# Performance work log

Measured on AMD Instinct MI355X. Metric: run time of the kernel, lower is better.

## Reference

```python
import jax, jax.numpy as jnp
import numpy as np

N = 50000
E = 600000
LLM_DIM = 640
HIDDEN = 128
STRUCT_DIM = 16
N_STRUCT_TYPES = 5
N_LAYERS = 2
LN_EPS = 1e-5


def setup_inputs() -> dict:
    key = jax.random.key(0)
    ks = jax.random.split(key, 10)
    llm_feat = jax.random.normal(ks[0], (N, LLM_DIM), dtype=jnp.float32)
    struct_type_ids = jax.random.randint(ks[1], (N,), 0, N_STRUCT_TYPES, dtype=jnp.int64)
    edge_index = jax.random.randint(ks[2], (2, E), 0, N, dtype=jnp.int64)
    proj_out = HIDDEN - STRUCT_DIM  # 112
    proj_W = jax.random.normal(ks[3], (LLM_DIM, proj_out), dtype=jnp.float32) / np.sqrt(LLM_DIM)
    proj_b = jnp.zeros((proj_out,), dtype=jnp.float32)
    struct_emb = jax.random.normal(ks[4], (N_STRUCT_TYPES, STRUCT_DIM), dtype=jnp.float32)
    gcn_W = jax.random.normal(ks[5], (N_LAYERS, HIDDEN, HIDDEN), dtype=jnp.float32) / np.sqrt(HIDDEN)
    gcn_b = jnp.zeros((N_LAYERS, HIDDEN), dtype=jnp.float32)
    ln_g = jnp.ones((HIDDEN,), dtype=jnp.float32)
    ln_b = jnp.zeros((HIDDEN,), dtype=jnp.float32)
    return dict(llm_feat=llm_feat, struct_type_ids=struct_type_ids, edge_index=edge_index,
                proj_W=proj_W, proj_b=proj_b, struct_emb=struct_emb,
                gcn_W=gcn_W, gcn_b=gcn_b, ln_g=ln_g, ln_b=ln_b)


def _gcn_conv(x, src, dst, deg_inv_sqrt, W, b):
    """PyG GCNConv: x' = D^{-1/2}(A+I)D^{-1/2} (x W) + b, D over A+I."""
    xw = x @ W  # [N, H]
    norm = deg_inv_sqrt[src] * deg_inv_sqrt[dst]  # [E]
    msg = xw[src] * norm[:, None]  # [E, H]
    agg = jax.ops.segment_sum(msg, dst, num_segments=N)  # [N, H]
    # self-loop contribution: norm_ii = deg_i^{-1}
    agg = agg + xw * (deg_inv_sqrt * deg_inv_sqrt)[:, None]
    return agg + b


def reference(llm_feat, struct_type_ids, edge_index, proj_W, proj_b,
              struct_emb, gcn_W, gcn_b, ln_g, ln_b):
    x_llm = llm_feat @ proj_W + proj_b  # [N, hidden-struct_dim]
    x_struct = struct_emb[struct_type_ids]  # [N, struct_dim]
    x = jnp.concatenate([x_llm, x_struct], axis=-1)  # [N, hidden]

    src, dst = edge_index[0], edge_index[1]
    # degree with self-loops (A + I)
    deg = 1.0 + jax.ops.segment_sum(jnp.ones((E,), dtype=x.dtype), dst, num_segments=N)
    deg_inv_sqrt = jax.lax.rsqrt(deg)

    for l in range(N_LAYERS):
        x_new = jax.nn.relu(_gcn_conv(x, src, dst, deg_inv_sqrt, gcn_W[l], gcn_b[l]))
        # dropout is identity in eval mode
        x = x + x_new

    mean = jnp.mean(x, axis=-1, keepdims=True)
    var = jnp.mean(jnp.square(x - mean), axis=-1, keepdims=True)
    return (x - mean) * jax.lax.rsqrt(var + LN_EPS) * ln_g + ln_b
```

## Files before the change

### kernel.cpp

```cpp
#include <hip/hip_runtime.h>

#define N_NODES 50000
#define E_EDGES 600000
#define LLM_DIM 640
#define HIDDEN 128
#define POUT 112
#define NB_SCAN 98
#define FILL_BLOCKS 2344
#define CONV_ELEMS (POUT * LLM_DIM + 2 * HIDDEN * HIDDEN)
#define CONV_BLOCKS 408

typedef __attribute__((ext_vector_type(8))) short bf16x8;
typedef __attribute__((ext_vector_type(4))) float f32x4;

__device__ inline unsigned short f2bf(float f) {
    unsigned u = __float_as_uint(f);
    u += 0x7fff + ((u >> 16) & 1);
    return (unsigned short)(u >> 16);
}
__device__ inline float bflo(unsigned v) { return __uint_as_float(v << 16); }
__device__ inline float bfhi(unsigned v) { return __uint_as_float(v & 0xffff0000u); }

__global__ void deg_count(const int* __restrict__ eidx, int* __restrict__ cnt) {
    int e = blockIdx.x * 256 + threadIdx.x;
    if (e < E_EDGES) atomicAdd(&cnt[eidx[E_EDGES + e]], 1);
}

__global__ __launch_bounds__(256) void scan_blocksum(const int* __restrict__ cnt, int* __restrict__ bsum,
                                                     float* __restrict__ dis) {
    __shared__ int s[256];
    int b = blockIdx.x, t = threadIdx.x;
    int i0 = b * 512 + t, i1 = i0 + 256;
    int c0 = (i0 < N_NODES ? cnt[i0] : 0);
    int c1 = (i1 < N_NODES ? cnt[i1] : 0);
    if (i0 < N_NODES) dis[i0] = rsqrtf(1.0f + (float)c0);
    if (i1 < N_NODES) dis[i1] = rsqrtf(1.0f + (float)c1);
    s[t] = c0 + c1;
    __syncthreads();
    for (int st = 128; st; st >>= 1) {
        if (t < st) s[t] += s[t + st];
        __syncthreads();
    }
    if (t == 0) bsum[b] = s[0];
}

__global__ void scan_bsum(const int* __restrict__ bsum, int* __restrict__ bpre) {
    __shared__ int s[128];
    int t = threadIdx.x;
    if (t < NB_SCAN) s[t] = bsum[t];
    __syncthreads();
    if (t == 0) {
        int a = 0;
        for (int i = 0; i < NB_SCAN; i++) { int v = s[i]; s[i] = a; a += v; }
    }
    __syncthreads();
    if (t < NB_SCAN) bpre[t] = s[t];
}

__global__ __launch_bounds__(256) void scan_offs(const int* __restrict__ cnt, const int* __restrict__ bpre,
                                                 int* __restrict__ offs) {
    __shared__ int sA[512], sB[512];
    int b = blockIdx.x, t = threadIdx.x;
    int i0 = b * 512 + t, i1 = i0 + 256;
    int v0 = (i0 < N_NODES ? cnt[i0] : 0);
    int v1 = (i1 < N_NODES ? cnt[i1] : 0);
    sA[t] = v0; sA[t + 256] = v1;
    int* src = sA; int* dst = sB;
    for (int st = 1; st < 512; st <<= 1) {
        __syncthreads();
        dst[t]       = src[t]       + (t       >= st ? src[t - st]       : 0);
        dst[t + 256] = src[t + 256] + (t + 256 >= st ? src[t + 256 - st] : 0);
        int* tmp = src; src = dst; dst = tmp;
    }
    __syncthreads();
    int base = bpre[b];
    if (i0 < N_NODES) offs[i0] = base + src[t] - v0;
    if (i1 < N_NODES) offs[i1] = base + src[t + 256] - v1;
    if (b == 0 && t == 0) offs[N_NODES] = E_EDGES;
}

__global__ void fill_and_conv(const int* __restrict__ eidx, const int* __restrict__ offs,
                              int* __restrict__ pos, int* __restrict__ srcs,
                              const float* __restrict__ Wp, const float* __restrict__ Wg,
                              unsigned short* __restrict__ Wt, unsigned short* __restrict__ Wt2) {
    int b = blockIdx.x;
    if (b < FILL_BLOCKS) {
        int e = b * 256 + threadIdx.x;
        if (e >= E_EDGES) return;
        int s = eidx[e];
        int d = eidx[E_EDGES + e];
        int p = atomicAdd(&pos[d], 1);
        srcs[offs[d] + p] = s;
    } else {
        int idx = (b - FILL_BLOCKS) * 256 + threadIdx.x;
        if (idx < POUT * LLM_DIM) {
            int n = idx / LLM_DIM;
            int k = idx - n * LLM_DIM;
            Wt[(size_t)n * LLM_DIM + k] = f2bf(Wp[(size_t)k * POUT + n]);
        } else if (idx < CONV_ELEMS) {
            int i2 = idx - POUT * LLM_DIM;
            int l = i2 >> 14;
            int rem = i2 & 16383;
            int n = rem >> 7;
            int k = rem & 127;
            Wt2[i2] = f2bf(Wg[l * 16384 + k * 128 + n]);
        }
    }
}

__global__ __launch_bounds__(256) void proj_mfma(const float* __restrict__ A,
                                                 const unsigned short* __restrict__ Wt,
                                                 const float* __restrict__ bias,
                                                 const float* __restrict__ emb,
                                                 const int* __restrict__ sid,
                                                 const float* __restrict__ dis,
                                                 unsigned short* __restrict__ Xs) {
    __shared__ short As[64][72];
    __shared__ short Bs[112][72];
    const int tid = threadIdx.x;
    const int wave = tid >> 6, lane = tid & 63;
    const int row0 = blockIdx.x * 64;
    const int l15 = lane & 15, l4 = lane >> 4;

    f32x4 acc[7];
#pragma unroll
    for (int j = 0; j < 7; j++) acc[j] = (f32x4){0.f, 0.f, 0.f, 0.f};

    for (int k0 = 0; k0 < LLM_DIM; k0 += 64) {
#pragma unroll
        for (int i = 0; i < 4; i++) {
            int f = i * 256 + tid;
            int r = f >> 4;
            int q = f & 15;
            int grow = row0 + r;
            float4 v = make_float4(0.f, 0.f, 0.f, 0.f);
            if (grow < N_NODES)
                v = *reinterpret_cast<const float4*>(A + (size_t)grow * LLM_DIM + k0 + q * 4);
            uint2 u;
            u.x = (unsigned)f2bf(v.x) | ((unsigned)f2bf(v.y) << 16);
            u.y = (unsigned)f2bf(v.z) | ((unsigned)f2bf(v.w) << 16);
            *reinterpret_cast<uint2*>(&As[r][q * 4]) = u;
        }
#pragma unroll
        for (int i = 0; i < 7; i++) {
            int f = i * 256 + tid;
            int n = f >> 4;
            int q = f & 15;
            uint2 v = *reinterpret_cast<const uint2*>(Wt + (size_t)n * LLM_DIM + k0 + q * 4);
            *reinterpret_cast<uint2*>(&Bs[n][q * 4]) = v;
        }
        __syncthreads();
#pragma unroll
        for (int ks = 0; ks < 2; ks++) {
            int kk = ks * 32 + l4 * 8;
            bf16x8 a = *reinterpret_cast<bf16x8*>(&As[wave * 16 + l15][kk]);
#pragma unroll
            for (int ct = 0; ct < 7; ct++) {
                bf16x8 b = *reinterpret_cast<bf16x8*>(&Bs[ct * 16 + l15][kk]);
                acc[ct] = __builtin_amdgcn_mfma_f32_16x16x32_bf16(a, b, acc[ct], 0, 0, 0);
            }
        }
        __syncthreads();
    }
#pragma unroll
    for (int r = 0; r < 4; r++) {
        int row = row0 + wave * 16 + l4 * 4 + r;
        if (row >= N_NODES) continue;
        float d = dis[row];
#pragma unroll
        for (int ct = 0; ct < 7; ct++) {
            int col = ct * 16 + l15;
            Xs[(size_t)row * HIDDEN + col] = f2bf(d * (acc[ct][r] + bias[col]));
        }
        float e = emb[sid[row] * 16 + l15];
        Xs[(size_t)row * HIDDEN + POUT + l15] = f2bf(d * e);
    }
}

__global__ __launch_bounds__(256) void gather(const unsigned short* __restrict__ Xs,
                                              const int* __restrict__ offs,
                                              const int* __restrict__ srcs,
                                              const float* __restrict__ dis,
                                              unsigned short* __restrict__ Gb) {
    int node = blockIdx.x * 4 + (threadIdx.x >> 6);
    int lane = threadIdx.x & 63;
    if (node >= N_NODES) return;
    int beg = __builtin_amdgcn_readfirstlane(offs[node]);
    int end = __builtin_amdgcn_readfirstlane(offs[node + 1]);
    const unsigned* X32 = reinterpret_cast<const unsigned*>(Xs);
    float d = dis[node];
    unsigned sv = X32[(size_t)node * 64 + lane];
    float ax = 0.f, ay = 0.f;
    int e = beg;
    while (e < end) {
        int n = end - e;
        if (n > 64) n = 64;
        int idx = (lane < n) ? srcs[e + lane] : 0;
        int j = 0;
        for (; j + 8 <= n; j += 8) {
            int s0 = __shfl(idx, j);
            int s1 = __shfl(idx, j + 1);
            int s2 = __shfl(idx, j + 2);
            int s3 = __shfl(idx, j + 3);
            int s4 = __shfl(idx, j + 4);
            int s5 = __shfl(idx, j + 5);
            int s6 = __shfl(idx, j + 6);
            int s7 = __shfl(idx, j + 7);
            unsigned v0 = X32[(size_t)s0 * 64 + lane];
            unsigned v1 = X32[(size_t)s1 * 64 + lane];
            unsigned v2 = X32[(size_t)s2 * 64 + lane];
            unsigned v3 = X32[(size_t)s3 * 64 + lane];
            unsigned v4 = X32[(size_t)s4 * 64 + lane];
            unsigned v5 = X32[(size_t)s5 * 64 + lane];
            unsigned v6 = X32[(size_t)s6 * 64 + lane];
            unsigned v7 = X32[(size_t)s7 * 64 + lane];
            ax += ((bflo(v0) + bflo(v1)) + (bflo(v2) + bflo(v3)))
                + ((bflo(v4) + bflo(v5)) + (bflo(v6) + bflo(v7)));
            ay += ((bfhi(v0) + bfhi(v1)) + (bfhi(v2) + bfhi(v3)))
                + ((bfhi(v4) + bfhi(v5)) + (bfhi(v6) + bfhi(v7)));
        }
        if (j + 4 <= n) {
            int s0 = __shfl(idx, j);
            int s1 = __shfl(idx, j + 1);
            int s2 = __shfl(idx, j + 2);
            int s3 = __shfl(idx, j + 3);
            unsigned v0 = X32[(size_t)s0 * 64 + lane];
            unsigned v1 = X32[(size_t)s1 * 64 + lane];
            unsigned v2 = X32[(size_t)s2 * 64 + lane];
            unsigned v3 = X32[(size_t)s3 * 64 + lane];
            ax += (bflo(v0) + bflo(v1)) + (bflo(v2) + bflo(v3));
            ay += (bfhi(v0) + bfhi(v1)) + (bfhi(v2) + bfhi(v3));
            j += 4;
        }
        int rem = n - j;
        if (rem > 0) {
            int s0 = __shfl(idx, j);
            int s1 = __shfl(idx, j + (rem > 1 ? 1 : 0));
            int s2 = __shfl(idx, j + (rem > 2 ? 2 : 0));
            unsigned v0 = X32[(size_t)s0 * 64 + lane];
            unsigned v1 = X32[(size_t)s1 * 64 + lane];
            unsigned v2 = X32[(size_t)s2 * 64 + lane];
            ax += bflo(v0) + (rem > 1 ? bflo(v1) : 0.f) + (rem > 2 ? bflo(v2) : 0.f);
            ay += bfhi(v0) + (rem > 1 ? bfhi(v1) : 0.f) + (rem > 2 ? bfhi(v2) : 0.f);
        }
        e += 64;
    }
    ax = d * (ax + bflo(sv));
    ay = d * (ay + bfhi(sv));
    reinterpret_cast<unsigned*>(Gb)[(size_t)node * 64 + lane] =
        (unsigned)f2bf(ax) | ((unsigned)f2bf(ay) << 16);
}

template <int MODE>
__global__ __launch_bounds__(256) void gemm_fin(const unsigned short* __restrict__ Gb,
                                                const unsigned short* __restrict__ Wt2,
                                                const float* __restrict__ bias,
                                                const float* __restrict__ dis,
                                                const float* __restrict__ lng,
                                                const float* __restrict__ lnb,
                                                const unsigned short* XsIn,
                                                float* __restrict__ X,
                                                unsigned short* XsOut) {
    __shared__ short As[64][136];
    __shared__ short Bs[128][136];
    const int tid = threadIdx.x;
    const int wave = tid >> 6, lane = tid & 63;
    const int row0 = blockIdx.x * 64;
    const int l15 = lane & 15, l4 = lane >> 4;

#pragma unroll
    for (int i = 0; i < 4; i++) {
        int f = i * 256 + tid;
        int r = f >> 4;
        int q = f & 15;
        int grow = row0 + r;
        uint4 v = make_uint4(0, 0, 0, 0);
        if (grow < N_NODES)
            v = reinterpret_cast<const uint4*>(Gb + (size_t)grow * HIDDEN)[q];
        *reinterpret_cast<uint4*>(&As[r][q * 8]) = v;
    }
#pragma unroll
    for (int i = 0; i < 8; i++) {
        int f = i * 256 + tid;
        int r = f >> 4;
        int q = f & 15;
        uint4 v = reinterpret_cast<const uint4*>(Wt2 + (size_t)r * HIDDEN)[q];
        *reinterpret_cast<uint4*>(&Bs[r][q * 8]) = v;
    }

    const unsigned* XsU = reinterpret_cast<const unsigned*>(XsIn);
    float xs[8][4];
    float dv[4];
#pragma unroll
    for (int r = 0; r < 4; r++) {
        int row = row0 + wave * 16 + l4 * 4 + r;
        int rc = row < N_NODES ? row : 0;
        dv[r] = dis[rc];
        bool hi = (l15 & 1) != 0;
#pragma unroll
        for (int ct = 0; ct < 8; ct++) {
            unsigned u = XsU[(size_t)rc * 64 + ct * 8 + (l15 >> 1)];
            xs[ct][r] = hi ? bfhi(u) : bflo(u);
        }
    }

    __syncthreads();

    f32x4 acc[8];
#pragma unroll
    for (int j = 0; j < 8; j++) acc[j] = (f32x4){0.f, 0.f, 0.f, 0.f};
#pragma unroll
    for (int ks = 0; ks < 4; ks++) {
        int kk = ks * 32 + l4 * 8;
        bf16x8 a = *reinterpret_cast<bf16x8*>(&As[wave * 16 + l15][kk]);
#pragma unroll
        for (int ct = 0; ct < 8; ct++) {
            bf16x8 b = *reinterpret_cast<bf16x8*>(&Bs[ct * 16 + l15][kk]);
            acc[ct] = __builtin_amdgcn_mfma_f32_16x16x32_bf16(a, b, acc[ct], 0, 0, 0);
        }
    }

    float bcol[8];
#pragma unroll
    for (int ct = 0; ct < 8; ct++) bcol[ct] = bias[ct * 16 + l15];

    float vv[8][4];
#pragma unroll
    for (int r = 0; r < 4; r++) {
#pragma unroll
        for (int ct = 0; ct < 8; ct++)
            vv[ct][r] = xs[ct][r] + dv[r] * fmaxf(acc[ct][r] + bcol[ct], 0.f);
    }

    if (MODE == 0) {
#pragma unroll
        for (int r = 0; r < 4; r++) {
            int row = row0 + wave * 16 + l4 * 4 + r;
            if (row >= N_NODES) continue;
#pragma unroll
            for (int ct = 0; ct < 8; ct++)
                XsOut[(size_t)row * HIDDEN + ct * 16 + l15] = f2bf(vv[ct][r]);
        }
    } else {
        float s[4], q2[4];
#pragma unroll
        for (int r = 0; r < 4; r++) {
            s[r] = 0.f; q2[r] = 0.f;
#pragma unroll
            for (int ct = 0; ct < 8; ct++) {
                s[r] += vv[ct][r];
                q2[r] += vv[ct][r] * vv[ct][r];
            }
        }
#pragma unroll
        for (int off = 1; off < 16; off <<= 1) {
#pragma unroll
            for (int r = 0; r < 4; r++) {
                s[r] += __shfl_xor(s[r], off);
                q2[r] += __shfl_xor(q2[r], off);
            }
        }
        float gcol[8], bcol2[8];
#pragma unroll
        for (int ct = 0; ct < 8; ct++) {
            gcol[ct] = lng[ct * 16 + l15];
            bcol2[ct] = lnb[ct * 16 + l15];
        }
#pragma unroll
        for (int r = 0; r < 4; r++) {
            int row = row0 + wave * 16 + l4 * 4 + r;
            if (row >= N_NODES) continue;
            float mean = s[r] * (1.f / 128.f);
            float var = q2[r] * (1.f / 128.f) - mean * mean;
            float inv = rsqrtf(var + 1e-5f * dv[r] * dv[r]);
#pragma unroll
            for (int ct = 0; ct < 8; ct++) {
                int col = ct * 16 + l15;
                X[(size_t)row * HIDDEN + col] = (vv[ct][r] - mean) * inv * gcol[ct] + bcol2[ct];
            }
        }
    }
}

extern "C" void kernel_launch(void* const* d_in, const int* in_sizes, int n_in,
                              void* d_out, int out_size, void* d_ws, size_t ws_size,
                              hipStream_t stream) {
    const float* llm   = (const float*)d_in[0];
    const int*   sid   = (const int*)d_in[1];
    const int*   eidx  = (const int*)d_in[2];
    const float* projW = (const float*)d_in[3];
    const float* projb = (const float*)d_in[4];
    const float* emb   = (const float*)d_in[5];
    const float* gcnW  = (const float*)d_in[6];
    const float* gcnb  = (const float*)d_in[7];
    const float* lng   = (const float*)d_in[8];
    const float* lnb   = (const float*)d_in[9];

    float* X = (float*)d_out;
    unsigned short* Xs = (unsigned short*)d_ws;
    unsigned short* Gb = Xs + (size_t)N_NODES * HIDDEN;
    unsigned short* Wt = Gb;
    unsigned short* Wt2 = Gb + (size_t)N_NODES * HIDDEN;
    float* dis = (float*)(Wt2 + 2 * HIDDEN * HIDDEN);
    int* cnt  = (int*)(dis + N_NODES);
    int* pos  = cnt + N_NODES;
    int* offs = pos + N_NODES;
    int* bsum = offs + N_NODES + 1;
    int* bpre = bsum + 128;
    int* srcs = bpre + 128;

    hipMemsetAsync(cnt, 0, 2 * N_NODES * sizeof(int), stream);
    deg_count<<<FILL_BLOCKS, 256, 0, stream>>>(eidx, cnt);
    scan_blocksum<<<NB_SCAN, 256, 0, stream>>>(cnt, bsum, dis);
    scan_bsum<<<1, 128, 0, stream>>>(bsum, bpre);
    scan_offs<<<NB_SCAN, 256, 0, stream>>>(cnt, bpre, offs);
    fill_and_conv<<<FILL_BLOCKS + CONV_BLOCKS, 256, 0, stream>>>(eidx, offs, pos, srcs,
                                                                 projW, gcnW, Wt, Wt2);

    proj_mfma<<<(N_NODES + 63) / 64, 256, 0, stream>>>(llm, Wt, projb, emb, sid, dis, Xs);

    gather<<<(N_NODES + 3) / 4, 256, 0, stream>>>(Xs, offs, srcs, dis, Gb);
    gemm_fin<0><<<(N_NODES + 63) / 64, 256, 0, stream>>>(Gb, Wt2, gcnb, dis, lng, lnb, Xs, X, Xs);
    gather<<<(N_NODES + 3) / 4, 256, 0, stream>>>(Xs, offs, srcs, dis, Gb);
    gemm_fin<1><<<(N_NODES + 63) / 64, 256, 0, stream>>>(Gb, Wt2 + HIDDEN * HIDDEN, gcnb + HIDDEN,
                                                         dis, lng, lnb, Xs, X, Xs);
}
```

Baseline: 364.5 us.

## Fuse CSR preprocessing kernels into one cooperative kernel with grid syncs

Replaces the memset plus five preprocessing kernels (degree count, block sums, prefix scan, fill, and weight conversion) with a single cooperative kernel of 256 blocks that separates phases with grid-wide syncs. This removes several kernel launch gaps and the memset call. In exchange, parallelism per phase drops to 256 grid-strided blocks, grid.sync carries its own cost, and the scan phases leave most blocks idle.

```diff
diff --git a/kernel.cpp b/kernel.cpp
--- a/kernel.cpp
+++ b/kernel.cpp
@@ -1,4 +1,7 @@
 #include <hip/hip_runtime.h>
+#include <hip/hip_cooperative_groups.h>
+
+namespace cg = cooperative_groups;
 
 #define N_NODES 50000
 #define E_EDGES 600000
@@ -6,9 +9,8 @@
 #define HIDDEN 128
 #define POUT 112
 #define NB_SCAN 98
-#define FILL_BLOCKS 2344
+#define PREP_BLOCKS 256
 #define CONV_ELEMS (POUT * LLM_DIM + 2 * HIDDEN * HIDDEN)
-#define CONV_BLOCKS 408
 
 typedef __attribute__((ext_vector_type(8))) short bf16x8;
 typedef __attribute__((ext_vector_type(4))) float f32x4;
@@ -21,84 +23,87 @@
 __device__ inline float bflo(unsigned v) { return __uint_as_float(v << 16); }
 __device__ inline float bfhi(unsigned v) { return __uint_as_float(v & 0xffff0000u); }
 
-__global__ void deg_count(const int* __restrict__ eidx, int* __restrict__ cnt) {
-    int e = blockIdx.x * 256 + threadIdx.x;
-    if (e < E_EDGES) atomicAdd(&cnt[eidx[E_EDGES + e]], 1);
-}
-
-__global__ __launch_bounds__(256) void scan_blocksum(const int* __restrict__ cnt, int* __restrict__ bsum,
-                                                     float* __restrict__ dis) {
-    __shared__ int s[256];
-    int b = blockIdx.x, t = threadIdx.x;
-    int i0 = b * 512 + t, i1 = i0 + 256;
-    int c0 = (i0 < N_NODES ? cnt[i0] : 0);
-    int c1 = (i1 < N_NODES ? cnt[i1] : 0);
-    if (i0 < N_NODES) dis[i0] = rsqrtf(1.0f + (float)c0);
-    if (i1 < N_NODES) dis[i1] = rsqrtf(1.0f + (float)c1);
-    s[t] = c0 + c1;
-    __syncthreads();
-    for (int st = 128; st; st >>= 1) {
-        if (t < st) s[t] += s[t + st];
-        __syncthreads();
-    }
-    if (t == 0) bsum[b] = s[0];
-}
-
-__global__ void scan_bsum(const int* __restrict__ bsum, int* __restrict__ bpre) {
-    __shared__ int s[128];
-    int t = threadIdx.x;
-    if (t < NB_SCAN) s[t] = bsum[t];
-    __syncthreads();
-    if (t == 0) {
-        int a = 0;
-        for (int i = 0; i < NB_SCAN; i++) { int v = s[i]; s[i] = a; a += v; }
-    }
-    __syncthreads();
-    if (t < NB_SCAN) bpre[t] = s[t];
-}
-
-__global__ __launch_bounds__(256) void scan_offs(const int* __restrict__ cnt, const int* __restrict__ bpre,
-                                                 int* __restrict__ offs) {
+__global__ __launch_bounds__(256) void prep_all(const int* __restrict__ eidx,
+                                                int* __restrict__ cnt, int* __restrict__ pos,
+                                                float* __restrict__ dis,
+                                                int* __restrict__ bsum, int* __restrict__ bpre,
+                                                int* __restrict__ offs, int* __restrict__ srcs,
+                                                const float* __restrict__ Wp, const float* __restrict__ Wg,
+                                                unsigned short* __restrict__ Wt,
+                                                unsigned short* __restrict__ Wt2) {
+    cg::grid_group grid = cg::this_grid();
     __shared__ int sA[512], sB[512];
-    int b = blockIdx.x, t = threadIdx.x;
-    int i0 = b * 512 + t, i1 = i0 + 256;
-    int v0 = (i0 < N_NODES ? cnt[i0] : 0);
-    int v1 = (i1 < N_NODES ? cnt[i1] : 0);
-    sA[t] = v0; sA[t + 256] = v1;
-    int* src = sA; int* dst = sB;
-    for (int st = 1; st < 512; st <<= 1) {
-        __syncthreads();
-        dst[t]       = src[t]       + (t       >= st ? src[t - st]       : 0);
-        dst[t + 256] = src[t + 256] + (t + 256 >= st ? src[t + 256 - st] : 0);
-        int* tmp = src; src = dst; dst = tmp;
-    }
-    __syncthreads();
-    int base = bpre[b];
-    if (i0 < N_NODES) offs[i0] = base + src[t] - v0;
-    if (i1 < N_NODES) offs[i1] = base + src[t + 256] - v1;
-    if (b == 0 && t == 0) offs[N_NODES] = E_EDGES;
-}
-
-__global__ void fill_and_conv(const int* __restrict__ eidx, const int* __restrict__ offs,
-                              int* __restrict__ pos, int* __restrict__ srcs,
-                              const float* __restrict__ Wp, const float* __restrict__ Wg,
-                              unsigned short* __restrict__ Wt, unsigned short* __restrict__ Wt2) {
-    int b = blockIdx.x;
-    if (b < FILL_BLOCKS) {
-        int e = b * 256 + threadIdx.x;
-        if (e >= E_EDGES) return;
-        int s = eidx[e];
-        int d = eidx[E_EDGES + e];
+    const int tid = threadIdx.x, b = blockIdx.x;
+    const int gtid = b * 256 + tid;
+    const int GT = PREP_BLOCKS * 256;
+
+    for (int i = gtid; i < 2 * N_NODES; i += GT) cnt[i] = 0;
+    grid.sync();
+
+    for (int e = gtid; e < E_EDGES; e += GT) atomicAdd(&cnt[eidx[E_EDGES + e]], 1);
+    grid.sync();
+
+    if (b < NB_SCAN) {
+        int i0 = b * 512 + tid, i1 = i0 + 256;
+        int c0 = (i0 < N_NODES ? cnt[i0] : 0);
+        int c1 = (i1 < N_NODES ? cnt[i1] : 0);
+        if (i0 < N_NODES) dis[i0] = rsqrtf(1.0f + (float)c0);
+        if (i1 < N_NODES) dis[i1] = rsqrtf(1.0f + (float)c1);
+        sA[tid] = c0 + c1;
+        __syncthreads();
+        for (int st = 128; st; st >>= 1) {
+            if (tid < st) sA[tid] += sA[tid + st];
+            __syncthreads();
+        }
+        if (tid == 0) bsum[b] = sA[0];
+    }
+    grid.sync();
+
+    if (b == 0) {
+        if (tid < NB_SCAN) sA[tid] = bsum[tid];
+        __syncthreads();
+        if (tid == 0) {
+            int a = 0;
+            for (int i = 0; i < NB_SCAN; i++) { int v = sA[i]; sA[i] = a; a += v; }
+        }
+        __syncthreads();
+        if (tid < NB_SCAN) bpre[tid] = sA[tid];
+    }
+    grid.sync();
+
+    if (b < NB_SCAN) {
+        int i0 = b * 512 + tid, i1 = i0 + 256;
+        int v0 = (i0 < N_NODES ? cnt[i0] : 0);
+        int v1 = (i1 < N_NODES ? cnt[i1] : 0);
+        sA[tid] = v0; sA[tid + 256] = v1;
+        int* src = sA; int* dst = sB;
+        for (int st = 1; st < 512; st <<= 1) {
+            __syncthreads();
+            dst[tid]       = src[tid]       + (tid       >= st ? src[tid - st]       : 0);
+            dst[tid + 256] = src[tid + 256] + (tid + 256 >= st ? src[tid + 256 - st] : 0);
+            int* tmp = src; src = dst; dst = tmp;
+        }
+        __syncthreads();
+        int base = bpre[b];
+        if (i0 < N_NODES) offs[i0] = base + src[tid] - v0;
+        if (i1 < N_NODES) offs[i1] = base + src[tid + 256] - v1;
+        if (b == 0 && tid == 0) offs[N_NODES] = E_EDGES;
+    }
+    grid.sync();
+
+    for (int e = gtid; e < E_EDGES; e += GT) {
+        int sn = eidx[e];
+        int d  = eidx[E_EDGES + e];
         int p = atomicAdd(&pos[d], 1);
-        srcs[offs[d] + p] = s;
-    } else {
-        int idx = (b - FILL_BLOCKS) * 256 + threadIdx.x;
-        if (idx < POUT * LLM_DIM) {
-            int n = idx / LLM_DIM;
-            int k = idx - n * LLM_DIM;
+        srcs[offs[d] + p] = sn;
+    }
+    for (int i = gtid; i < CONV_ELEMS; i += GT) {
+        if (i < POUT * LLM_DIM) {
+            int n = i / LLM_DIM;
+            int k = i - n * LLM_DIM;
             Wt[(size_t)n * LLM_DIM + k] = f2bf(Wp[(size_t)k * POUT + n]);
-        } else if (idx < CONV_ELEMS) {
-            int i2 = idx - POUT * LLM_DIM;
+        } else {
+            int i2 = i - POUT * LLM_DIM;
             int l = i2 >> 14;
             int rem = i2 & 16383;
             int n = rem >> 7;
@@ -409,13 +414,10 @@
     int* bpre = bsum + 128;
     int* srcs = bpre + 128;
 
-    hipMemsetAsync(cnt, 0, 2 * N_NODES * sizeof(int), stream);
-    deg_count<<<FILL_BLOCKS, 256, 0, stream>>>(eidx, cnt);
-    scan_blocksum<<<NB_SCAN, 256, 0, stream>>>(cnt, bsum, dis);
-    scan_bsum<<<1, 128, 0, stream>>>(bsum, bpre);
-    scan_offs<<<NB_SCAN, 256, 0, stream>>>(cnt, bpre, offs);
-    fill_and_conv<<<FILL_BLOCKS + CONV_BLOCKS, 256, 0, stream>>>(eidx, offs, pos, srcs,
-                                                                 projW, gcnW, Wt, Wt2);
+    void* args[] = {(void*)&eidx, (void*)&cnt, (void*)&pos, (void*)&dis,
+                    (void*)&bsum, (void*)&bpre, (void*)&offs, (void*)&srcs,
+                    (void*)&projW, (void*)&gcnW, (void*)&Wt, (void*)&Wt2};
+    hipLaunchCooperativeKernel((void*)prep_all, dim3(PREP_BLOCKS), dim3(256), args, 0, stream);
 
     proj_mfma<<<(N_NODES + 63) / 64, 256, 0, stream>>>(llm, Wt, projb, emb, sid, dis, Xs);
 
```

New measurement: 510.6 us. 40.1% more time.
